# Kernel tuning notes

Measured on AMD Instinct MI355X. Metric: run time of the kernel, lower is better.

Reference implementation:

```python
import jax, jax.numpy as jnp
import numpy as np

V, D, H, L, F, B, S = 512, 512, 8, 6, 2048, 8, 1024
DK = D // H
EPS = 1e-5


def _positional_encoding(max_len, d_model):
    pos = np.arange(max_len, dtype=np.float32)[:, None]
    div = np.exp(np.arange(0, d_model, 2, dtype=np.float32) * (-np.log(10000.0) / d_model))
    pe = np.zeros((max_len, d_model), dtype=np.float32)
    pe[:, 0::2] = np.sin(pos * div)
    pe[:, 1::2] = np.cos(pos * div)
    return jnp.asarray(pe)


def setup_inputs() -> dict:
    key = jax.random.key(0)
    ks = jax.random.split(key, 24)
    xavier = lambda k, shp: jax.random.normal(k, shp, jnp.float32) * np.sqrt(2.0 / (shp[-2] + shp[-1]))
    inp = {
        "input_ids": jax.random.randint(ks[0], (B, S), 0, V),
        "emb": jax.random.normal(ks[1], (V, D), jnp.float32) * 0.02,
        "pe": _positional_encoding(1024, D),
        "Wq": xavier(ks[2], (L, D, D)), "bq": jnp.zeros((L, D)),
        "Wk": xavier(ks[3], (L, D, D)), "bk": jnp.zeros((L, D)),
        "Wv": xavier(ks[4], (L, D, D)), "bv": jnp.zeros((L, D)),
        "Wo": xavier(ks[5], (L, D, D)), "bo": jnp.zeros((L, D)),
        "ln1_g": jnp.ones((L, D)), "ln1_b": jnp.zeros((L, D)),
        "W1": xavier(ks[6], (L, D, F)), "b1": jnp.zeros((L, F)),
        "W2": xavier(ks[7], (L, F, D)), "b2": jnp.zeros((L, D)),
        "ln2_g": jnp.ones((L, D)), "ln2_b": jnp.zeros((L, D)),
        "Wout": xavier(ks[8], (D, V)), "bout": jnp.zeros((V,)),
    }
    return inp


def _ln(x, g, b):
    mu = jnp.mean(x, -1, keepdims=True)
    var = jnp.mean(jnp.square(x - mu), -1, keepdims=True)
    return (x - mu) * jax.lax.rsqrt(var + EPS) * g + b


def reference(input_ids, emb, pe, Wq, bq, Wk, bk, Wv, bv, Wo, bo,
              ln1_g, ln1_b, W1, b1, W2, b2, ln2_g, ln2_b, Wout, bout):
    h = emb[input_ids] * np.sqrt(D) + pe[:S]  # [B,S,D]
    # Faithful to the original mask bug: masked_fill(mask==0, -1e9) fills the
    # LOWER triangle (incl diagonal); raw scores are kept strictly where j > i.
    r = jnp.arange(S)
    keep = r[None, :] > r[:, None]  # [S,S]

    def block(h, p):
        (wq, bq_, wk, bk_, wv, bv_, wo, bo_,
         g1, be1, w1, b1_, w2, b2_, g2, be2) = p
        split = lambda t: t.reshape(B, S, H, DK).transpose(0, 2, 1, 3)
        q = split(h @ wq + bq_)
        k = split(h @ wk + bk_)
        v = split(h @ wv + bv_)
        scores = jnp.einsum('bhqd,bhkd->bhqk', q, k) / np.sqrt(DK)
        scores = jnp.where(keep, scores, -1e9)
        a = jax.nn.softmax(scores, axis=-1)
        o = jnp.einsum('bhqk,bhkd->bhqd', a, v).transpose(0, 2, 1, 3).reshape(B, S, D)
        h = _ln(h + (o @ wo + bo_), g1, be1)
        f = jax.nn.relu(h @ w1 + b1_) @ w2 + b2_
        h = _ln(h + f, g2, be2)
        return h, None

    params = (Wq, bq, Wk, bk, Wv, bv, Wo, bo, ln1_g, ln1_b, W1, b1, W2, b2, ln2_g, ln2_b)
    h, _ = jax.lax.scan(block, h, params)
    return h @ Wout + bout  # logits [B,S,V]
```

## Files before the change

kernel.cpp:

```cpp
#include <hip/hip_runtime.h>

typedef unsigned short u16;
typedef __attribute__((ext_vector_type(8))) short bf16x8;
typedef __attribute__((ext_vector_type(4))) float f32x4;
typedef __attribute__((ext_vector_type(4))) unsigned int uint4v;
typedef __attribute__((ext_vector_type(4))) unsigned short us4;

#define NLAYER 6
#define D_MODEL 512
#define NHEAD 8
#define DKH 64
#define SEQ 1024
#define BATCH 8
#define FFN 2048
#define MROWS (BATCH * SEQ)
#define QKV_LD 1536
#define SCALE_LOG2E 0.18033688011112042f

__device__ __forceinline__ float b2f(u16 u) {
  union { unsigned u32; float f; } x; x.u32 = ((unsigned)u) << 16; return x.f;
}
__device__ __forceinline__ u16 f2b(float f) {
  union { float f; unsigned u; } x; x.f = f;
  unsigned r = x.u + 0x7FFFu + ((x.u >> 16) & 1u);
  return (u16)(r >> 16);
}
__device__ __forceinline__ void gld16(const u16* g, u16* l) {
  __builtin_amdgcn_global_load_lds(
      (const __attribute__((address_space(1))) unsigned int*)g,
      (__attribute__((address_space(3))) unsigned int*)l, 16, 0, 0);
}

__global__ __launch_bounds__(256) void transpose_cvt_kernel(
    const float* __restrict__ src, u16* __restrict__ dst, int K, int N, size_t dstZ,
    float scale)
{
  __shared__ float t[32][33];
  const int z = blockIdx.z;
  src += (size_t)z * K * N;
  dst += (size_t)z * dstZ;
  const int n0 = blockIdx.x * 32, k0 = blockIdx.y * 32;
  const int tx = threadIdx.x, ty = threadIdx.y;
#pragma unroll
  for (int i = 0; i < 32; i += 8)
    t[ty + i][tx] = src[(size_t)(k0 + ty + i) * N + n0 + tx];
  __syncthreads();
#pragma unroll
  for (int i = 0; i < 32; i += 8)
    dst[(size_t)(n0 + ty + i) * K + k0 + tx] = f2b(t[tx][ty + i] * scale);
}

__global__ __launch_bounds__(256) void concat_bias_kernel(
    const float* __restrict__ bq, const float* __restrict__ bk,
    const float* __restrict__ bv, float* __restrict__ dst)
{
  const int l = blockIdx.x, t = threadIdx.x;
#pragma unroll
  for (int j = t; j < 512; j += 256) {
    dst[l * QKV_LD + j]        = bq[l * 512 + j] * SCALE_LOG2E;
    dst[l * QKV_LD + 512 + j]  = bk[l * 512 + j];
    dst[l * QKV_LD + 1024 + j] = bv[l * 512 + j];
  }
}

__global__ __launch_bounds__(256) void embed_kernel(
    const int* __restrict__ ids, const float* __restrict__ emb,
    const float* __restrict__ pe, float* __restrict__ Hf, u16* __restrict__ Hb)
{
  const int row = blockIdx.x;
  const int s = row & (SEQ - 1);
  const int id = ids[row];
  const int tid = threadIdx.x;
#pragma unroll
  for (int u = 0; u < 2; ++u) {
    const int d = tid + u * 256;
    float v = emb[(size_t)id * D_MODEL + d] * 22.62741699796952f + pe[(size_t)s * D_MODEL + d];
    Hf[(size_t)row * D_MODEL + d] = v;
    Hb[(size_t)row * D_MODEL + d] = f2b(v);
  }
}

template<int BMT, bool RELU, bool OUTF, bool OUTB, bool VT>
__global__ __launch_bounds__(256) void gemm_kernel(
    const u16* __restrict__ A, const u16* __restrict__ Bt,
    const float* __restrict__ bias,
    float* __restrict__ Cf, u16* __restrict__ Cb, u16* __restrict__ Vtp,
    int M, int N, int K)
{
  constexpr int IT = BMT / 32;
  __shared__ __align__(16) u16 As[BMT * 32];
  __shared__ __align__(16) u16 Bs[128 * 32];
  const int tid = threadIdx.x;
  const int bm = blockIdx.x * BMT, bn = blockIdx.y * 128;
  const int wave = tid >> 6, lane = tid & 63;
  const int lm = lane & 15, quad = lane >> 4;
  const int wm = (wave & 1) * (BMT / 2), wn = (wave >> 1) * 64;
  const int r0 = tid >> 2;
  const int c0 = (tid & 3) * 8;

  const u16* Ap = A  + (size_t)(bm + r0) * K + c0;
  const u16* Bp = Bt + (size_t)(bn + r0) * K + c0;
  u16* lA  = As + wave * 512;
  u16* lA2 = lA + 64 * 32;
  u16* lB  = Bs + wave * 512;
  u16* lB2 = lB + 64 * 32;

  f32x4 acc[IT][4] = {};

  for (int kk = 0; kk < K; kk += 32) {
    __syncthreads();
    gld16(Ap + kk, lA);
    if (BMT == 128) gld16(Ap + kk + (size_t)64 * K, lA2);
    gld16(Bp + kk, lB);
    gld16(Bp + kk + (size_t)64 * K, lB2);
    __syncthreads();
    bf16x8 af[IT], bg[4];
#pragma unroll
    for (int i = 0; i < IT; ++i)
      af[i] = *(const bf16x8*)&As[(wm + i * 16 + lm) * 32 + quad * 8];
#pragma unroll
    for (int j = 0; j < 4; ++j)
      bg[j] = *(const bf16x8*)&Bs[(wn + j * 16 + lm) * 32 + quad * 8];
#pragma unroll
    for (int i = 0; i < IT; ++i)
#pragma unroll
      for (int j = 0; j < 4; ++j)
        acc[i][j] = __builtin_amdgcn_mfma_f32_16x16x32_bf16(af[i], bg[j], acc[i][j], 0, 0, 0);
  }

  const int mbase = bm + wm + quad * 4;
  const int nbase = bn + wn + lm;
#pragma unroll
  for (int i = 0; i < IT; ++i) {
#pragma unroll
    for (int j = 0; j < 4; ++j) {
      const int n = nbase + j * 16;
      const float bv = bias[n];
      float vv[4];
#pragma unroll
      for (int r = 0; r < 4; ++r) {
        float v = acc[i][j][r] + bv;
        if (RELU) v = fmaxf(v, 0.f);
        vv[r] = v;
      }
      if (VT && n >= 1024) {
        const int hh = (n - 1024) >> 6, d = (n - 1024) & 63;
        const int mm = mbase + i * 16;
        const int bb = mm >> 10, ss = mm & 1023;
        us4 pk;
#pragma unroll
        for (int r = 0; r < 4; ++r) pk[r] = f2b(vv[r]);
        *(us4*)&Vtp[(((size_t)(bb * NHEAD + hh)) * 64 + d) * SEQ + ss] = pk;
      } else {
#pragma unroll
        for (int r = 0; r < 4; ++r) {
          const int m = mbase + i * 16 + r;
          if (OUTF) Cf[(size_t)m * N + n] = vv[r];
          if (OUTB) Cb[(size_t)m * N + n] = f2b(vv[r]);
        }
      }
    }
  }
}

__global__ __launch_bounds__(256) void attn_mfma_kernel(
    const u16* __restrict__ QKV, const u16* __restrict__ Vt, u16* __restrict__ O)
{
  __shared__ __align__(16) u16 Ks[64 * 64];
  __shared__ __align__(16) u16 Vs[64 * 64];
  __shared__ __align__(16) u16 Ps[4 * 16 * 64];
  const int tid = threadIdx.x;
  const int wave = tid >> 6, lane = tid & 63;
  const int quad = lane >> 4, l15 = lane & 15;
  const int l7 = l15 & 7;
  const int id = blockIdx.x;
  const int bh = id & 63;
  const int b = bh >> 3, h = bh & 7;
  const int g = id >> 6;
  const int u = g * 4 + wave;
  u16* psw = Ps + wave * (16 * 64);
  const size_t qoff = (size_t)b * SEQ * QKV_LD + h * 64;
  const size_t vtb  = (size_t)bh * 64 * SEQ;

  const int sr = tid >> 3, sc = tid & 7;
  const u16* kg0 = QKV + qoff + 512 + (size_t)sr * QKV_LD + sc * 8;
  const u16* kg1 = kg0 + (size_t)32 * QKV_LD;
  const u16* vg0 = Vt + vtb + (size_t)sr * SEQ + sc * 8;
  const u16* vg1 = vg0 + (size_t)32 * SEQ;
  const int sw = (sc ^ (sr & 7)) << 3;
  u16* ks0 = &Ks[sr * 64 + sw];
  u16* ks1 = &Ks[(sr + 32) * 64 + sw];
  u16* vs0 = &Vs[sr * 64 + sw];
  u16* vs1 = &Vs[(sr + 32) * 64 + sw];

  const u16* qp = QKV + qoff + (size_t)(u * 16 + l15) * QKV_LD + quad * 8;
  const bf16x8 qf0 = *(const bf16x8*)(qp);
  const bf16x8 qf1 = *(const bf16x8*)(qp + 32);

  f32x4 oacc[4] = {};
  float lsum[4] = {0.f, 0.f, 0.f, 0.f};

  uint4v kr0 = *(const uint4v*)(kg0 + (size_t)(g * 64) * QKV_LD);
  uint4v kr1 = *(const uint4v*)(kg1 + (size_t)(g * 64) * QKV_LD);
  uint4v vr0 = *(const uint4v*)(vg0 + g * 64);
  uint4v vr1 = *(const uint4v*)(vg1 + g * 64);

#pragma unroll 1
  for (int jt = g; jt < 16; ++jt) {
    __syncthreads();
    *(uint4v*)ks0 = kr0; *(uint4v*)ks1 = kr1;
    *(uint4v*)vs0 = vr0; *(uint4v*)vs1 = vr1;
    __syncthreads();
    if (jt < 15) {
      kr0 = *(const uint4v*)(kg0 + (size_t)((jt + 1) * 64) * QKV_LD);
      kr1 = *(const uint4v*)(kg1 + (size_t)((jt + 1) * 64) * QKV_LD);
      vr0 = *(const uint4v*)(vg0 + (jt + 1) * 64);
      vr1 = *(const uint4v*)(vg1 + (jt + 1) * 64);
    }
    f32x4 sacc[4] = {};
#pragma unroll
    for (int nt = 0; nt < 4; ++nt) {
      const int key = nt * 16 + l15, k7 = key & 7;
      bf16x8 kb0 = *(const bf16x8*)&Ks[key * 64 + ((quad ^ k7) << 3)];
      bf16x8 kb1 = *(const bf16x8*)&Ks[key * 64 + (((quad + 4) ^ k7) << 3)];
      sacc[nt] = __builtin_amdgcn_mfma_f32_16x16x32_bf16(qf0, kb0, sacc[nt], 0, 0, 0);
      sacc[nt] = __builtin_amdgcn_mfma_f32_16x16x32_bf16(qf1, kb1, sacc[nt], 0, 0, 0);
    }
    const bool diag = (jt == g);
#pragma unroll
    for (int nt = 0; nt < 4; ++nt)
#pragma unroll
      for (int r = 0; r < 4; ++r) {
        float pv = __builtin_amdgcn_exp2f(sacc[nt][r]);
        if (diag) {
          const int i = u * 16 + quad * 4 + r;
          const int j = jt * 64 + nt * 16 + l15;
          pv = (j > i) ? pv : 0.f;
        }
        lsum[r] += pv;
        const int qr = quad * 4 + r;
        const int j2 = nt * 16 + l15;
        psw[qr * 64 + (((j2 >> 3) ^ (qr & 7)) << 3) + (j2 & 7)] = f2b(pv);
      }
    bf16x8 pf0 = *(const bf16x8*)&psw[l15 * 64 + (((quad + 0) ^ l7) << 3)];
    bf16x8 pf1 = *(const bf16x8*)&psw[l15 * 64 + (((quad + 4) ^ l7) << 3)];
#pragma unroll
    for (int nt = 0; nt < 4; ++nt) {
      const int d = nt * 16 + l15, d7 = d & 7;
      bf16x8 vb0 = *(const bf16x8*)&Vs[d * 64 + ((quad ^ d7) << 3)];
      bf16x8 vb1 = *(const bf16x8*)&Vs[d * 64 + (((quad + 4) ^ d7) << 3)];
      oacc[nt] = __builtin_amdgcn_mfma_f32_16x16x32_bf16(pf0, vb0, oacc[nt], 0, 0, 0);
      oacc[nt] = __builtin_amdgcn_mfma_f32_16x16x32_bf16(pf1, vb1, oacc[nt], 0, 0, 0);
    }
  }

#pragma unroll
  for (int o = 1; o < 16; o <<= 1)
#pragma unroll
    for (int r = 0; r < 4; ++r) lsum[r] += __shfl_xor(lsum[r], o, 16);
  float rl[4];
#pragma unroll
  for (int r = 0; r < 4; ++r) rl[r] = 1.0f / lsum[r];
#pragma unroll
  for (int nt = 0; nt < 4; ++nt)
#pragma unroll
    for (int r = 0; r < 4; ++r) {
      const int row = u * 16 + quad * 4 + r;
      O[(size_t)(b * SEQ + row) * D_MODEL + h * DKH + nt * 16 + l15] = f2b(oacc[nt][r] * rl[r]);
    }
}

__global__ __launch_bounds__(256) void vmean_kernel(
    const u16* __restrict__ Vt, u16* __restrict__ O)
{
  const int bh = blockIdx.x, tid = threadIdx.x;
  const int d = tid >> 2, sc = (tid & 3) * 256;
  const u16* p = Vt + ((size_t)bh * 64 + d) * SEQ + sc;
  float s = 0.f;
#pragma unroll 8
  for (int i = 0; i < 256; ++i) s += b2f(p[i]);
  s += __shfl_xor(s, 1, 64);
  s += __shfl_xor(s, 2, 64);
  if ((tid & 3) == 0) {
    const int b = bh >> 3, h = bh & 7;
    O[((size_t)b * SEQ + SEQ - 1) * D_MODEL + h * 64 + d] = f2b(s * (1.f / SEQ));
  }
}

__global__ __launch_bounds__(256) void add_ln_kernel(
    const float* __restrict__ Hin, const u16* __restrict__ T,
    const float* __restrict__ g, const float* __restrict__ bta,
    float* __restrict__ Hout, u16* __restrict__ Hb)
{
  __shared__ float red[8];
  const int row = blockIdx.x, tid = threadIdx.x;
  const int wave = tid >> 6, lane = tid & 63;
  const size_t base = (size_t)row * D_MODEL;
  const float x0 = Hin[base + tid] + b2f(T[base + tid]);
  const float x1 = Hin[base + tid + 256] + b2f(T[base + tid + 256]);
  float s = x0 + x1;
#pragma unroll
  for (int o = 32; o > 0; o >>= 1) s += __shfl_xor(s, o, 64);
  if (lane == 0) red[wave] = s;
  __syncthreads();
  const float mu = (red[0] + red[1] + red[2] + red[3]) * (1.f / 512.f);
  const float d0 = x0 - mu, d1 = x1 - mu;
  float v = d0 * d0 + d1 * d1;
#pragma unroll
  for (int o = 32; o > 0; o >>= 1) v += __shfl_xor(v, o, 64);
  if (lane == 0) red[4 + wave] = v;
  __syncthreads();
  const float var = (red[4] + red[5] + red[6] + red[7]) * (1.f / 512.f);
  const float rs = rsqrtf(var + 1e-5f);
  const float y0 = d0 * rs * g[tid] + bta[tid];
  const float y1 = d1 * rs * g[tid + 256] + bta[tid + 256];
  Hout[base + tid] = y0;
  Hout[base + tid + 256] = y1;
  Hb[base + tid] = f2b(y0);
  Hb[base + tid + 256] = f2b(y1);
}

extern "C" void kernel_launch(void* const* d_in, const int* in_sizes, int n_in,
                              void* d_out, int out_size, void* d_ws, size_t ws_size,
                              hipStream_t stream) {
  (void)in_sizes; (void)n_in; (void)out_size; (void)ws_size;
  const int*   ids  = (const int*)  d_in[0];
  const float* emb  = (const float*)d_in[1];
  const float* pe   = (const float*)d_in[2];
  const float* Wq   = (const float*)d_in[3];
  const float* bq   = (const float*)d_in[4];
  const float* Wk   = (const float*)d_in[5];
  const float* bk   = (const float*)d_in[6];
  const float* Wv   = (const float*)d_in[7];
  const float* bv   = (const float*)d_in[8];
  const float* Wo   = (const float*)d_in[9];
  const float* bo   = (const float*)d_in[10];
  const float* g1   = (const float*)d_in[11];
  const float* be1  = (const float*)d_in[12];
  const float* W1   = (const float*)d_in[13];
  const float* b1   = (const float*)d_in[14];
  const float* W2   = (const float*)d_in[15];
  const float* b2   = (const float*)d_in[16];
  const float* g2   = (const float*)d_in[17];
  const float* be2  = (const float*)d_in[18];
  const float* Wout = (const float*)d_in[19];
  const float* bout = (const float*)d_in[20];
  float* out = (float*)d_out;

  char* wsp = (char*)d_ws;
  auto alloc = [&](size_t bytes) -> char* {
    char* p = wsp; wsp += (bytes + 255) & ~(size_t)255; return p;
  };
  const size_t dd  = (size_t)D_MODEL * D_MODEL;
  const size_t df  = (size_t)D_MODEL * FFN;
  const size_t dq  = (size_t)QKV_LD * D_MODEL;
  u16* wqkv_t = (u16*)alloc(NLAYER * dq * 2);
  u16* wo_t   = (u16*)alloc(NLAYER * dd * 2);
  u16* w1_t   = (u16*)alloc(NLAYER * df * 2);
  u16* w2_t   = (u16*)alloc(NLAYER * df * 2);
  u16* wout_t = (u16*)alloc(dd * 2);
  float* bqkv = (float*)alloc(NLAYER * QKV_LD * 4);
  float* hf   = (float*)alloc((size_t)MROWS * D_MODEL * 4);
  u16*   hb   = (u16*)  alloc((size_t)MROWS * D_MODEL * 2);
  u16*   qkvb = (u16*)  alloc((size_t)MROWS * QKV_LD * 2);
  u16*   ob   = (u16*)  alloc((size_t)MROWS * D_MODEL * 2);
  u16*   vt   = (u16*)  alloc((size_t)BATCH * NHEAD * DKH * SEQ * 2);
  u16*   tb   = (u16*)  alloc((size_t)MROWS * D_MODEL * 2);
  u16*   mid  = qkvb;

  dim3 tb8(32, 8);
  transpose_cvt_kernel<<<dim3(16, 16, NLAYER), tb8, 0, stream>>>(Wq, wqkv_t,            512, 512,  dq, SCALE_LOG2E);
  transpose_cvt_kernel<<<dim3(16, 16, NLAYER), tb8, 0, stream>>>(Wk, wqkv_t + 512*512,  512, 512,  dq, 1.f);
  transpose_cvt_kernel<<<dim3(16, 16, NLAYER), tb8, 0, stream>>>(Wv, wqkv_t + 1024*512, 512, 512,  dq, 1.f);
  transpose_cvt_kernel<<<dim3(16, 16, NLAYER), tb8, 0, stream>>>(Wo, wo_t,   512, 512,  dd, 1.f);
  transpose_cvt_kernel<<<dim3(64, 16, NLAYER), tb8, 0, stream>>>(W1, w1_t,   512, 2048, df, 1.f);
  transpose_cvt_kernel<<<dim3(16, 64, NLAYER), tb8, 0, stream>>>(W2, w2_t,   2048, 512, df, 1.f);
  transpose_cvt_kernel<<<dim3(16, 16, 1),      tb8, 0, stream>>>(Wout, wout_t, 512, 512, dd, 1.f);
  concat_bias_kernel<<<NLAYER, 256, 0, stream>>>(bq, bk, bv, bqkv);

  embed_kernel<<<MROWS, 256, 0, stream>>>(ids, emb, pe, hf, hb);

  for (int l = 0; l < NLAYER; ++l) {
    gemm_kernel<128, false, false, true, true><<<dim3(64, 12), 256, 0, stream>>>(
        hb, wqkv_t + l * dq, bqkv + l * QKV_LD, nullptr, qkvb, vt, MROWS, QKV_LD, 512);
    attn_mfma_kernel<<<1024, 256, 0, stream>>>(qkvb, vt, ob);
    vmean_kernel<<<64, 256, 0, stream>>>(vt, ob);
    gemm_kernel<64, false, false, true, false><<<dim3(128, 4), 256, 0, stream>>>(
        ob, wo_t + l * dd, bo + l * 512, nullptr, tb, nullptr, MROWS, 512, 512);
    add_ln_kernel<<<MROWS, 256, 0, stream>>>(hf, tb, g1 + l * 512, be1 + l * 512, hf, hb);
    gemm_kernel<128, true, false, true, false><<<dim3(64, 16), 256, 0, stream>>>(
        hb, w1_t + l * df, b1 + l * 2048, nullptr, mid, nullptr, MROWS, 2048, 512);
    gemm_kernel<64, false, false, true, false><<<dim3(128, 4), 256, 0, stream>>>(
        mid, w2_t + l * df, b2 + l * 512, nullptr, tb, nullptr, MROWS, 512, 2048);
    add_ln_kernel<<<MROWS, 256, 0, stream>>>(hf, tb, g2 + l * 512, be2 + l * 512, hf, hb);
  }
  gemm_kernel<64, false, true, false, false><<<dim3(128, 4), 256, 0, stream>>>(
      hb, wout_t, bout, out, nullptr, nullptr, MROWS, 512, 512);
}
```

Before: 1.134 ms.

## Double-buffer GEMM LDS tiles with K=64 steps and XOR swizzle

Restructures the GEMM main loop to prefetch the next K tile into a second LDS buffer while the current one feeds MFMA. It widens the K step from 32 to 64, which halves the number of barriers per tile, and XOR-swizzles the LDS layout to avoid bank conflicts on fragment reads. The cost is four times the LDS footprint, which may lower occupancy. It also relies on gld16 async loads completing before the barrier.

```diff
diff --git a/kernel.cpp b/kernel.cpp
--- a/kernel.cpp
+++ b/kernel.cpp
@@ -88,44 +88,64 @@
     int M, int N, int K)
 {
   constexpr int IT = BMT / 32;
-  __shared__ __align__(16) u16 As[BMT * 32];
-  __shared__ __align__(16) u16 Bs[128 * 32];
+  constexpr int AHALF = BMT * 64;
+  constexpr int BHALF = 128 * 64;
+  __shared__ __align__(16) u16 As[2 * AHALF];
+  __shared__ __align__(16) u16 Bs[2 * BHALF];
   const int tid = threadIdx.x;
   const int bm = blockIdx.x * BMT, bn = blockIdx.y * 128;
   const int wave = tid >> 6, lane = tid & 63;
   const int lm = lane & 15, quad = lane >> 4;
   const int wm = (wave & 1) * (BMT / 2), wn = (wave >> 1) * 64;
-  const int r0 = tid >> 2;
-  const int c0 = (tid & 3) * 8;
-
-  const u16* Ap = A  + (size_t)(bm + r0) * K + c0;
-  const u16* Bp = Bt + (size_t)(bn + r0) * K + c0;
-  u16* lA  = As + wave * 512;
-  u16* lA2 = lA + 64 * 32;
-  u16* lB  = Bs + wave * 512;
-  u16* lB2 = lB + 64 * 32;
+
+  const int sr = tid >> 3;
+  const int sc = (tid & 7) ^ (sr & 7);
+  const u16* Ap = A  + (size_t)(bm + sr) * K + sc * 8;
+  const u16* Bp = Bt + (size_t)(bn + sr) * K + sc * 8;
+  u16* lA = As + wave * 512;
+  u16* lB = Bs + wave * 512;
 
   f32x4 acc[IT][4] = {};
 
-  for (int kk = 0; kk < K; kk += 32) {
+  const int nt = K >> 6;
+  auto stage = [&](int buf, int t) {
+    const size_t ko = (size_t)t << 6;
+#pragma unroll
+    for (int p = 0; p < BMT / 32; ++p)
+      gld16(Ap + (size_t)(p * 32) * K + ko, lA + buf * AHALF + p * 2048);
+#pragma unroll
+    for (int p = 0; p < 4; ++p)
+      gld16(Bp + (size_t)(p * 32) * K + ko, lB + buf * BHALF + p * 2048);
+  };
+
+  stage(0, 0);
+  __syncthreads();
+
+  for (int t = 0; t < nt; ++t) {
+    const int cur = t & 1;
+    if (t + 1 < nt) stage(cur ^ 1, t + 1);
+    const u16* as = As + cur * AHALF;
+    const u16* bs = Bs + cur * BHALF;
+#pragma unroll
+    for (int kh = 0; kh < 2; ++kh) {
+      bf16x8 af[IT], bg[4];
+#pragma unroll
+      for (int i = 0; i < IT; ++i) {
+        const int row = wm + i * 16 + lm;
+        af[i] = *(const bf16x8*)&as[row * 64 + (((kh * 4 + quad) ^ (row & 7)) << 3)];
+      }
+#pragma unroll
+      for (int j = 0; j < 4; ++j) {
+        const int row = wn + j * 16 + lm;
+        bg[j] = *(const bf16x8*)&bs[row * 64 + (((kh * 4 + quad) ^ (row & 7)) << 3)];
+      }
+#pragma unroll
+      for (int i = 0; i < IT; ++i)
+#pragma unroll
+        for (int j = 0; j < 4; ++j)
+          acc[i][j] = __builtin_amdgcn_mfma_f32_16x16x32_bf16(af[i], bg[j], acc[i][j], 0, 0, 0);
+    }
     __syncthreads();
-    gld16(Ap + kk, lA);
-    if (BMT == 128) gld16(Ap + kk + (size_t)64 * K, lA2);
-    gld16(Bp + kk, lB);
-    gld16(Bp + kk + (size_t)64 * K, lB2);
-    __syncthreads();
-    bf16x8 af[IT], bg[4];
-#pragma unroll
-    for (int i = 0; i < IT; ++i)
-      af[i] = *(const bf16x8*)&As[(wm + i * 16 + lm) * 32 + quad * 8];
-#pragma unroll
-    for (int j = 0; j < 4; ++j)
-      bg[j] = *(const bf16x8*)&Bs[(wn + j * 16 + lm) * 32 + quad * 8];
-#pragma unroll
-    for (int i = 0; i < IT; ++i)
-#pragma unroll
-      for (int j = 0; j < 4; ++j)
-        acc[i][j] = __builtin_amdgcn_mfma_f32_16x16x32_bf16(af[i], bg[j], acc[i][j], 0, 0, 0);
   }
 
   const int mbase = bm + wm + quad * 4;
```

New measurement: 1.046 ms. 7.7% less time.
